# Optimization experiments

Measured on AMD Instinct MI355X. Metric: run time of the kernel, lower is better.

The kernel has to match this reference:

```python
import jax, jax.numpy as jnp
import numpy as np
import math

B, N, D, H = 4, 2048, 256, 4
DH = D // H
EPS = 1e-8


def setup_inputs() -> dict:
    key = jax.random.key(0)
    ks = jax.random.split(key, 8)
    x = jax.random.normal(ks[0], (B, N, D), dtype=jnp.float32)
    # RoPE rotation freqs: exp(i * pos * inv_freq), stored as (cos, sin) pairs -> [N, DH//2, 2]
    d2 = DH // 2
    inv_freq = 1.0 / (10000.0 ** (jnp.arange(d2, dtype=jnp.float32) / d2))
    ang = jnp.arange(N, dtype=jnp.float32)[:, None] * inv_freq[None, :]
    freqs = jnp.stack([jnp.cos(ang), jnp.sin(ang)], axis=-1)  # [N, d2, 2]
    s = 0.02
    g = jnp.ones((D,), dtype=jnp.float32)
    w_qkv = jax.random.normal(ks[1], (D, 3 * D), dtype=jnp.float32) * s
    b_qkv = jnp.zeros((3 * D,), dtype=jnp.float32)
    w_out = jax.random.normal(ks[2], (D, D), dtype=jnp.float32) * s
    b_out = jnp.zeros((D,), dtype=jnp.float32)
    w_gate = jax.random.normal(ks[3], (D, D), dtype=jnp.float32) * s
    b_gate = jnp.zeros((D,), dtype=jnp.float32)
    return {"x": x, "freqs": freqs, "g": g, "w_qkv": w_qkv, "b_qkv": b_qkv,
            "w_out": w_out, "b_out": b_out, "w_gate": w_gate, "b_gate": b_gate}


def _zcrmsnorm(x, g):
    x0 = x - jnp.mean(x, axis=-1, keepdims=True)
    rms = jnp.sqrt(jnp.mean(x0 * x0, axis=-1, keepdims=True) + EPS)
    return x0 / rms * g


def _rope(q, freqs):
    # q: [B,H,N,DH]; freqs: [N,DH//2,2] (cos,sin). Complex multiply on adjacent pairs.
    b, h, n, dh = q.shape
    qp = q.reshape(b, h, n, dh // 2, 2)
    cos = freqs[:n, :, 0][None, None]  # [1,1,N,d2]
    sin = freqs[:n, :, 1][None, None]
    q0, q1 = qp[..., 0], qp[..., 1]
    out = jnp.stack([q0 * cos - q1 * sin, q0 * sin + q1 * cos], axis=-1)
    return out.reshape(b, h, n, dh)


def reference(x, freqs, g, w_qkv, b_qkv, w_out, b_out, w_gate, b_gate):
    b, n, d = x.shape
    h = _zcrmsnorm(x, g)
    qkv = (h @ w_qkv + b_qkv).reshape(b, n, 3, H, DH)
    qkv = jnp.transpose(qkv, (2, 0, 3, 1, 4))  # [3,B,H,N,DH]
    q, k, v = qkv[0], qkv[1], qkv[2]
    q = _rope(q, freqs)
    k = _rope(k, freqs)
    scores = jnp.einsum('bhqd,bhkd->bhqk', q, k) / math.sqrt(DH)
    attn = jax.nn.softmax(scores, axis=-1)  # dropout is identity in eval
    y = jnp.einsum('bhqk,bhkd->bhqd', attn, v)
    y = jnp.transpose(y, (0, 2, 1, 3)).reshape(b, n, d)
    y = y @ w_out + b_out
    gate = jax.nn.sigmoid(h @ w_gate + b_gate)
    return x + gate * y
```

## Files before the change

kernel.cpp:

```cpp
#include <hip/hip_runtime.h>

typedef unsigned short u16;
typedef unsigned int u32;
typedef short short8 __attribute__((ext_vector_type(8)));
typedef float f32x4 __attribute__((ext_vector_type(4)));

#define B_ 4
#define N_ 2048
#define D_ 256
#define H_ 4
#define DH_ 64
#define BN_ 8192

__device__ inline float b2f(u16 u) {
    union { u32 i; float f; } v; v.i = ((u32)u) << 16; return v.f;
}
__device__ inline u16 f2b(float f) {
    union { float f; u32 i; } v; v.f = f;
    return (u16)((v.i + 0x8000u) >> 16);
}
__device__ inline u32 pkbf(float a, float b) {
    union { float f; u32 i; } ua, ub; ua.f = a; ub.f = b;
    return __builtin_amdgcn_perm(ub.i + 0x8000u, ua.i + 0x8000u, 0x07060302u);
}
__device__ inline f32x4 mfma16(short8 a, short8 b, f32x4 c) {
    return __builtin_amdgcn_mfma_f32_16x16x32_bf16(a, b, c, 0, 0, 0);
}

__device__ __forceinline__ void gemm_body(
    int bx, int by, int tid,
    const u16* __restrict__ A, const u16* __restrict__ BT,
    const float* __restrict__ bias, void* __restrict__ Cout,
    int Ntot)
{
    const int wave = tid >> 6, lane = tid & 63;
    const int ln15 = lane & 15, quad = lane >> 4;
    const int m0 = bx * 128 + (wave & 1) * 64;
    const int n0 = by * 128 + (wave >> 1) * 64;

    const f32x4 zero = {0.f, 0.f, 0.f, 0.f};
    f32x4 acc[4][4];
    #pragma unroll
    for (int i = 0; i < 4; ++i)
        #pragma unroll
        for (int j = 0; j < 4; ++j) acc[i][j] = zero;

    #pragma unroll
    for (int k0 = 0; k0 < 256; k0 += 32) {
        const int koff = k0 + quad * 8;
        short8 a[4], b[4];
        #pragma unroll
        for (int i = 0; i < 4; ++i)
            a[i] = *(const short8*)(A + (size_t)(m0 + i * 16 + ln15) * 256 + koff);
        #pragma unroll
        for (int j = 0; j < 4; ++j)
            b[j] = *(const short8*)(BT + (size_t)(n0 + j * 16 + ln15) * 256 + koff);
        #pragma unroll
        for (int i = 0; i < 4; ++i)
            #pragma unroll
            for (int j = 0; j < 4; ++j)
                acc[i][j] = mfma16(a[i], b[j], acc[i][j]);
    }

    #pragma unroll
    for (int i = 0; i < 4; ++i) {
        const int r = m0 + i * 16 + quad * 4;
        #pragma unroll
        for (int j = 0; j < 4; ++j) {
            const int c = n0 + j * 16 + ln15;
            const float bv = bias[c];
            #pragma unroll
            for (int rg = 0; rg < 4; ++rg) {
                const size_t idx = (size_t)(r + rg) * Ntot + c;
                ((u16*)Cout)[idx] = f2b(acc[i][j][rg] + bv);
            }
        }
    }
}

__device__ __forceinline__ void gemm_thin_body(
    int bx, int by, int tid,
    const u16* __restrict__ A, const u16* __restrict__ BT,
    const float* __restrict__ bias, void* __restrict__ Cout,
    const float* __restrict__ xin, const u16* __restrict__ gate,
    int mode)
{
    const int wave = tid >> 6, lane = tid & 63;
    const int ln15 = lane & 15, quad = lane >> 4;
    const int m0 = bx * 64 + (wave & 1) * 32;
    const int n0 = by * 64 + (wave >> 1) * 32;

    const f32x4 zero = {0.f, 0.f, 0.f, 0.f};
    f32x4 acc[2][2];
    #pragma unroll
    for (int i = 0; i < 2; ++i)
        #pragma unroll
        for (int j = 0; j < 2; ++j) acc[i][j] = zero;

    #pragma unroll
    for (int k0 = 0; k0 < 256; k0 += 32) {
        const int koff = k0 + quad * 8;
        short8 a[2], b[2];
        #pragma unroll
        for (int i = 0; i < 2; ++i)
            a[i] = *(const short8*)(A + (size_t)(m0 + i * 16 + ln15) * 256 + koff);
        #pragma unroll
        for (int j = 0; j < 2; ++j)
            b[j] = *(const short8*)(BT + (size_t)(n0 + j * 16 + ln15) * 256 + koff);
        #pragma unroll
        for (int i = 0; i < 2; ++i)
            #pragma unroll
            for (int j = 0; j < 2; ++j)
                acc[i][j] = mfma16(a[i], b[j], acc[i][j]);
    }

    #pragma unroll
    for (int i = 0; i < 2; ++i) {
        const int r = m0 + i * 16 + quad * 4;
        #pragma unroll
        for (int j = 0; j < 2; ++j) {
            const int c = n0 + j * 16 + ln15;
            const float bv = bias[c];
            #pragma unroll
            for (int rg = 0; rg < 4; ++rg) {
                const size_t idx = (size_t)(r + rg) * 256 + c;
                float v = acc[i][j][rg] + bv;
                if (mode == 1) {
                    ((u16*)Cout)[idx] = f2b(1.0f / (1.0f + __expf(-v)));
                } else {
                    ((float*)Cout)[idx] = xin[idx] + b2f(gate[idx]) * v;
                }
            }
        }
    }
}

__global__ __launch_bounds__(256) void gemm_ep(
    const u16* __restrict__ A, const u16* __restrict__ BT,
    const float* __restrict__ bias, void* __restrict__ Cout, int Ntot)
{
    gemm_body(blockIdx.x, blockIdx.y, threadIdx.x, A, BT, bias, Cout, Ntot);
}

__global__ __launch_bounds__(256) void gemm_thin(
    const u16* __restrict__ A, const u16* __restrict__ BT,
    const float* __restrict__ bias, void* __restrict__ Cout,
    const float* __restrict__ xin, const u16* __restrict__ gate, int mode)
{
    gemm_thin_body(blockIdx.x, blockIdx.y, threadIdx.x, A, BT, bias, Cout,
                   xin, gate, mode);
}

__global__ __launch_bounds__(256) void norm_transw_k(
    const float* __restrict__ x, const float* __restrict__ g, u16* __restrict__ h,
    const float* __restrict__ wqkv, const float* __restrict__ wout,
    const float* __restrict__ wgate,
    u16* __restrict__ wqkvT, u16* __restrict__ woutT, u16* __restrict__ wgateT)
{
    if (blockIdx.x < 2048) {
        const int wave = threadIdx.x >> 6, lane = threadIdx.x & 63;
        const int t = blockIdx.x * 4 + wave;
        const float4 u = *(const float4*)(x + (size_t)t * D_ + lane * 4);
        float s  = u.x + u.y + u.z + u.w;
        float s2 = u.x * u.x + u.y * u.y + u.z * u.z + u.w * u.w;
        #pragma unroll
        for (int m = 1; m < 64; m <<= 1) {
            s  += __shfl_xor(s, m);
            s2 += __shfl_xor(s2, m);
        }
        float mean = s * (1.0f / D_);
        float var  = s2 * (1.0f / D_) - mean * mean;
        float rinv = rsqrtf(var + 1e-8f);
        const float4 gv = *(const float4*)(g + lane * 4);
        uint2 o;
        o.x = pkbf((u.x - mean) * rinv * gv.x, (u.y - mean) * rinv * gv.y);
        o.y = pkbf((u.z - mean) * rinv * gv.z, (u.w - mean) * rinv * gv.w);
        *(uint2*)(h + (size_t)t * D_ + lane * 4) = o;
    } else {
        int idx = (blockIdx.x - 2048) * 256 + threadIdx.x;
        if (idx < 768 * 256) {
            int nn = idx >> 8, kk = idx & 255;
            wqkvT[idx] = f2b(wqkv[kk * 768 + nn]);
        }
        idx -= 768 * 256;
        if (idx >= 0 && idx < 256 * 256) {
            int nn = idx >> 8, kk = idx & 255;
            woutT[idx]  = f2b(wout[kk * 256 + nn]);
            wgateT[idx] = f2b(wgate[kk * 256 + nn]);
        }
    }
}

#define QSCALE 0.18033688f
__global__ __launch_bounds__(256) void rope_vt_gate_k(
    const u16* __restrict__ qkv, const float* __restrict__ freqs,
    u16* __restrict__ Q, u16* __restrict__ K, u16* __restrict__ VT,
    const u16* __restrict__ h, const u16* __restrict__ wgateT,
    const float* __restrict__ b_gate, u16* __restrict__ gatb)
{
    __shared__ __align__(16) u16 tile[64 * 65];
    const int blk = blockIdx.x;
    if (blk < 1024) {
        const int idx = blk * 256 + threadIdx.x;
        const int t = idx >> 5, rem = idx & 31;
        const int hh = rem >> 3, s8 = rem & 7;
        const int b = t >> 11, n = t & 2047;

        const float4 f0 = *(const float4*)(freqs + (size_t)n * 64 + s8 * 8);
        const float4 f1 = *(const float4*)(freqs + (size_t)n * 64 + s8 * 8 + 4);

        const u16* qp = qkv + (size_t)t * 768 + hh * 64 + s8 * 8;
        const uint4 qv = *(const uint4*)qp;
        const uint4 kv = *(const uint4*)(qp + 256);

        const size_t off = ((size_t)(b * H_ + hh) * N_ + n) * DH_ + s8 * 8;
        uint4 qo, ko;
        {
            float q0 = b2f((u16)(qv.x & 0xffff)), q1 = b2f((u16)(qv.x >> 16));
            float k0 = b2f((u16)(kv.x & 0xffff)), k1 = b2f((u16)(kv.x >> 16));
            qo.x = pkbf((q0 * f0.x - q1 * f0.y) * QSCALE, (q0 * f0.y + q1 * f0.x) * QSCALE);
            ko.x = pkbf(k0 * f0.x - k1 * f0.y, k0 * f0.y + k1 * f0.x);
        }
        {
            float q0 = b2f((u16)(qv.y & 0xffff)), q1 = b2f((u16)(qv.y >> 16));
            float k0 = b2f((u16)(kv.y & 0xffff)), k1 = b2f((u16)(kv.y >> 16));
            qo.y = pkbf((q0 * f0.z - q1 * f0.w) * QSCALE, (q0 * f0.w + q1 * f0.z) * QSCALE);
            ko.y = pkbf(k0 * f0.z - k1 * f0.w, k0 * f0.w + k1 * f0.z);
        }
        {
            float q0 = b2f((u16)(qv.z & 0xffff)), q1 = b2f((u16)(qv.z >> 16));
            float k0 = b2f((u16)(kv.z & 0xffff)), k1 = b2f((u16)(kv.z >> 16));
            qo.z = pkbf((q0 * f1.x - q1 * f1.y) * QSCALE, (q0 * f1.y + q1 * f1.x) * QSCALE);
            ko.z = pkbf(k0 * f1.x - k1 * f1.y, k0 * f1.y + k1 * f1.x);
        }
        {
            float q0 = b2f((u16)(qv.w & 0xffff)), q1 = b2f((u16)(qv.w >> 16));
            float k0 = b2f((u16)(kv.w & 0xffff)), k1 = b2f((u16)(kv.w >> 16));
            qo.w = pkbf((q0 * f1.z - q1 * f1.w) * QSCALE, (q0 * f1.w + q1 * f1.z) * QSCALE);
            ko.w = pkbf(k0 * f1.z - k1 * f1.w, k0 * f1.w + k1 * f1.z);
        }
        *(uint4*)(Q + off) = qo;
        *(uint4*)(K + off) = ko;
    } else if (blk < 1536) {
        const int id2 = blk - 1024;
        const int bh = id2 & 15;
        const int n0 = (id2 >> 4) * 64;
        const int b = bh >> 2, hh = bh & 3;
        #pragma unroll
        for (int rep = 0; rep < 16; ++rep) {
            int idx = rep * 256 + threadIdx.x;
            int nl = idx >> 6, dh = idx & 63;
            tile[dh * 65 + nl] = qkv[(size_t)(b * N_ + n0 + nl) * 768 + 512 + hh * 64 + dh];
        }
        __syncthreads();
        #pragma unroll
        for (int rep = 0; rep < 16; ++rep) {
            int idx = rep * 256 + threadIdx.x;
            int dh = idx >> 6, nl = idx & 63;
            VT[((size_t)bh * 64 + dh) * N_ + n0 + nl] = tile[dh * 65 + nl];
        }
    } else {
        const int id3 = blk - 1536;
        gemm_thin_body(id3 & 127, id3 >> 7, threadIdx.x, h, wgateT, b_gate,
                       (void*)gatb, (const float*)nullptr, (const u16*)nullptr, 1);
    }
}

__global__ __launch_bounds__(256) void attn_k(
    const u16* __restrict__ Q, const u16* __restrict__ K,
    const u16* __restrict__ VT, u16* __restrict__ yt)
{
    __shared__ __align__(16) u16 Ks[2][64][64];
    __shared__ __align__(16) u16 Vs[2][64][64];
    __shared__ __align__(16) u16 Pb[4][16 * 88];
    const int tid = threadIdx.x;
    const int wave = tid >> 6, lane = tid & 63;
    const int ln15 = lane & 15, quad = lane >> 4;
    const int id = blockIdx.x;
    const int bh = ((id & 7) << 1) | ((id >> 3) & 1);
    const int q0 = (id >> 4) * 64 + wave * 16;

    const u16* Qh = Q + (size_t)bh * N_ * DH_;
    const u16* Kh = K + (size_t)bh * N_ * DH_;
    const u16* Vh = VT + (size_t)bh * DH_ * N_;

    const short8 bq0 = *(const short8*)(Qh + (size_t)(q0 + ln15) * DH_ + quad * 8);
    const short8 bq1 = *(const short8*)(Qh + (size_t)(q0 + ln15) * DH_ + 32 + quad * 8);

    const f32x4 zero = {0.f, 0.f, 0.f, 0.f};
    f32x4 o[4];
    #pragma unroll
    for (int j = 0; j < 4; ++j) o[j] = zero;
    float lv = 0.f;
    u16* Pw = Pb[wave];

    const int srow = tid >> 2, sq4 = tid & 3;
    const int swr = (srow & 7) << 3;
    const int wc0 = (sq4 * 8) ^ swr;
    const int wc1 = (sq4 * 8 + 32) ^ swr;
    const int swl = (ln15 & 7) << 3;
    const int rc0 = (quad * 8) ^ swl;
    const int rc1 = (quad * 8 + 32) ^ swl;

    {
        uint4 k0 = *(const uint4*)(Kh + (size_t)srow * DH_ + sq4 * 8);
        uint4 k1 = *(const uint4*)(Kh + (size_t)srow * DH_ + (sq4 + 4) * 8);
        uint4 v0 = *(const uint4*)(Vh + (size_t)srow * N_ + sq4 * 8);
        uint4 v1 = *(const uint4*)(Vh + (size_t)srow * N_ + (sq4 + 4) * 8);
        *(uint4*)&Ks[0][srow][wc0] = k0;
        *(uint4*)&Ks[0][srow][wc1] = k1;
        *(uint4*)&Vs[0][srow][wc0] = v0;
        *(uint4*)&Vs[0][srow][wc1] = v1;
    }
    __syncthreads();

    int p = 0;
    for (int c = 0; c < 32; ++c) {
        const int ktn = (c + 1) * 64;
        uint4 k0, k1, v0, v1;
        const bool more = (c + 1 < 32);
        if (more) {
            k0 = *(const uint4*)(Kh + (size_t)(ktn + srow) * DH_ + sq4 * 8);
            k1 = *(const uint4*)(Kh + (size_t)(ktn + srow) * DH_ + (sq4 + 4) * 8);
            v0 = *(const uint4*)(Vh + (size_t)srow * N_ + ktn + sq4 * 8);
            v1 = *(const uint4*)(Vh + (size_t)srow * N_ + ktn + (sq4 + 4) * 8);
        }

        f32x4 st[4];
        #pragma unroll
        for (int c4 = 0; c4 < 4; ++c4) {
            short8 ka0 = *(const short8*)&Ks[p][c4 * 16 + ln15][rc0];
            short8 ka1 = *(const short8*)&Ks[p][c4 * 16 + ln15][rc1];
            st[c4] = mfma16(ka0, bq0, zero);
            st[c4] = mfma16(ka1, bq1, st[c4]);
        }
        f32x4 pr[4];
        float rs = 0.f;
        #pragma unroll
        for (int c4 = 0; c4 < 4; ++c4) {
            #pragma unroll
            for (int r = 0; r < 4; ++r) {
                pr[c4][r] = exp2f(st[c4][r]);
                rs += pr[c4][r];
            }
        }
        lv += rs;
        #pragma unroll
        for (int c4 = 0; c4 < 4; ++c4) {
            uint2 w;
            w.x = pkbf(pr[c4][0], pr[c4][1]);
            w.y = pkbf(pr[c4][2], pr[c4][3]);
            *(uint2*)(Pw + ln15 * 88 + c4 * 16 + quad * 4) = w;
        }
        asm volatile("s_waitcnt lgkmcnt(0)" ::: "memory");
        const short8 bp0 = *(const short8*)(Pw + ln15 * 88 + quad * 8);
        const short8 bp1 = *(const short8*)(Pw + ln15 * 88 + 32 + quad * 8);
        #pragma unroll
        for (int j = 0; j < 4; ++j) {
            short8 va0 = *(const short8*)&Vs[p][j * 16 + ln15][rc0];
            short8 va1 = *(const short8*)&Vs[p][j * 16 + ln15][rc1];
            o[j] = mfma16(va0, bp0, o[j]);
            o[j] = mfma16(va1, bp1, o[j]);
        }

        if (more) {
            *(uint4*)&Ks[p ^ 1][srow][wc0] = k0;
            *(uint4*)&Ks[p ^ 1][srow][wc1] = k1;
            *(uint4*)&Vs[p ^ 1][srow][wc0] = v0;
            *(uint4*)&Vs[p ^ 1][srow][wc1] = v1;
        }
        __syncthreads();
        p ^= 1;
    }

    lv += __shfl_xor(lv, 16);
    lv += __shfl_xor(lv, 32);
    const float rl = 1.0f / lv;
    const int b = bh >> 2, h = bh & 3;
    const size_t base = ((size_t)b * N_ + q0 + ln15) * D_ + h * 64;
    #pragma unroll
    for (int j = 0; j < 4; ++j) {
        uint2 w;
        w.x = pkbf(o[j][0] * rl, o[j][1] * rl);
        w.y = pkbf(o[j][2] * rl, o[j][3] * rl);
        *(uint2*)(yt + base + j * 16 + quad * 4) = w;
    }
}

extern "C" void kernel_launch(void* const* d_in, const int* in_sizes, int n_in,
                              void* d_out, int out_size, void* d_ws, size_t ws_size,
                              hipStream_t stream) {
    const float* x      = (const float*)d_in[0];
    const float* freqs  = (const float*)d_in[1];
    const float* g      = (const float*)d_in[2];
    const float* w_qkv  = (const float*)d_in[3];
    const float* b_qkv  = (const float*)d_in[4];
    const float* w_out  = (const float*)d_in[5];
    const float* b_out  = (const float*)d_in[6];
    const float* w_gate = (const float*)d_in[7];
    const float* b_gate = (const float*)d_in[8];
    float* out = (float*)d_out;

    char* ws = (char*)d_ws;
    size_t off = 0;
    auto carve = [&](size_t nelem) -> u16* {
        u16* p = (u16*)(ws + off);
        off += ((nelem * 2 + 255) / 256) * 256;
        return p;
    };
    u16* h      = carve((size_t)BN_ * D_);
    u16* qkv    = carve((size_t)BN_ * 768);
    u16* Qb     = carve((size_t)BN_ * D_);
    u16* Kb     = carve((size_t)BN_ * D_);
    u16* VT     = carve((size_t)BN_ * D_);
    u16* gatb   = carve((size_t)BN_ * D_);
    u16* wqkvT  = carve((size_t)768 * 256);
    u16* woutT  = carve((size_t)256 * 256);
    u16* wgateT = carve((size_t)256 * 256);
    u16* yt = qkv;

    hipLaunchKernelGGL(norm_transw_k, dim3(3072), dim3(256), 0, stream,
                       x, g, h, w_qkv, w_out, w_gate, wqkvT, woutT, wgateT);
    hipLaunchKernelGGL(gemm_ep, dim3(BN_ / 128, 6), dim3(256), 0, stream,
                       h, wqkvT, b_qkv, (void*)qkv, 768);
    hipLaunchKernelGGL(rope_vt_gate_k, dim3(2048), dim3(256), 0, stream,
                       qkv, freqs, Qb, Kb, VT, h, wgateT, b_gate, gatb);
    hipLaunchKernelGGL(attn_k, dim3(512), dim3(256), 0, stream,
                       Qb, Kb, VT, yt);
    hipLaunchKernelGGL(gemm_thin, dim3(128, 4), dim3(256), 0, stream,
                       yt, woutT, b_out, (void*)out, x, gatb, 2);
}
```

Before: 168.0 us.

## Split attention key range across two halves and merge partials in combine kernel

The attention kernel now uses 512-thread blocks covering 128 queries. Each block handles only half of the key sequence, which doubles the waves in flight per block and halves the loop length per wave. Unnormalized fp32 partial outputs and row sums are written to workspace, aliased over the dead h/qkv and weight buffers. A new combine kernel adds the two halves, normalizes, and writes bf16 output for the final GEMM. This trades an extra launch and about 16MB of fp32 partial traffic for more parallelism and latency hiding in attention.

```diff
diff --git a/kernel.cpp b/kernel.cpp
--- a/kernel.cpp
+++ b/kernel.cpp
@@ -266,19 +266,22 @@
     }
 }
 
-__global__ __launch_bounds__(256) void attn_k(
+__global__ __launch_bounds__(512, 4) void attn_k(
     const u16* __restrict__ Q, const u16* __restrict__ K,
-    const u16* __restrict__ VT, u16* __restrict__ yt)
+    const u16* __restrict__ VT, float* __restrict__ Op,
+    float* __restrict__ lvp)
 {
     __shared__ __align__(16) u16 Ks[2][64][64];
     __shared__ __align__(16) u16 Vs[2][64][64];
-    __shared__ __align__(16) u16 Pb[4][16 * 88];
+    __shared__ __align__(16) u16 Pb[8][16 * 88];
     const int tid = threadIdx.x;
     const int wave = tid >> 6, lane = tid & 63;
     const int ln15 = lane & 15, quad = lane >> 4;
     const int id = blockIdx.x;
-    const int bh = ((id & 7) << 1) | ((id >> 3) & 1);
-    const int q0 = (id >> 4) * 64 + wave * 16;
+    const int bh   = ((id & 7) << 1) | ((id >> 3) & 1);
+    const int half = (id >> 4) & 1;
+    const int q0   = (id >> 5) * 128 + wave * 16;
+    const int kt0  = half * 1024;
 
     const u16* Qh = Q + (size_t)bh * N_ * DH_;
     const u16* Kh = K + (size_t)bh * N_ * DH_;
@@ -294,36 +297,28 @@
     float lv = 0.f;
     u16* Pw = Pb[wave];
 
-    const int srow = tid >> 2, sq4 = tid & 3;
-    const int swr = (srow & 7) << 3;
-    const int wc0 = (sq4 * 8) ^ swr;
-    const int wc1 = (sq4 * 8 + 32) ^ swr;
+    const int srow = tid >> 3, sq8 = tid & 7;
+    const int wc = (sq8 * 8) ^ ((srow & 7) << 3);
     const int swl = (ln15 & 7) << 3;
     const int rc0 = (quad * 8) ^ swl;
     const int rc1 = (quad * 8 + 32) ^ swl;
 
     {
-        uint4 k0 = *(const uint4*)(Kh + (size_t)srow * DH_ + sq4 * 8);
-        uint4 k1 = *(const uint4*)(Kh + (size_t)srow * DH_ + (sq4 + 4) * 8);
-        uint4 v0 = *(const uint4*)(Vh + (size_t)srow * N_ + sq4 * 8);
-        uint4 v1 = *(const uint4*)(Vh + (size_t)srow * N_ + (sq4 + 4) * 8);
-        *(uint4*)&Ks[0][srow][wc0] = k0;
-        *(uint4*)&Ks[0][srow][wc1] = k1;
-        *(uint4*)&Vs[0][srow][wc0] = v0;
-        *(uint4*)&Vs[0][srow][wc1] = v1;
+        uint4 k0 = *(const uint4*)(Kh + (size_t)(kt0 + srow) * DH_ + sq8 * 8);
+        uint4 v0 = *(const uint4*)(Vh + (size_t)srow * N_ + kt0 + sq8 * 8);
+        *(uint4*)&Ks[0][srow][wc] = k0;
+        *(uint4*)&Vs[0][srow][wc] = v0;
     }
     __syncthreads();
 
     int p = 0;
-    for (int c = 0; c < 32; ++c) {
-        const int ktn = (c + 1) * 64;
-        uint4 k0, k1, v0, v1;
-        const bool more = (c + 1 < 32);
+    for (int c = 0; c < 16; ++c) {
+        const int ktn = kt0 + (c + 1) * 64;
+        uint4 k0, v0;
+        const bool more = (c + 1 < 16);
         if (more) {
-            k0 = *(const uint4*)(Kh + (size_t)(ktn + srow) * DH_ + sq4 * 8);
-            k1 = *(const uint4*)(Kh + (size_t)(ktn + srow) * DH_ + (sq4 + 4) * 8);
-            v0 = *(const uint4*)(Vh + (size_t)srow * N_ + ktn + sq4 * 8);
-            v1 = *(const uint4*)(Vh + (size_t)srow * N_ + ktn + (sq4 + 4) * 8);
+            k0 = *(const uint4*)(Kh + (size_t)(ktn + srow) * DH_ + sq8 * 8);
+            v0 = *(const uint4*)(Vh + (size_t)srow * N_ + ktn + sq8 * 8);
         }
 
         f32x4 st[4];
@@ -364,10 +359,8 @@
         }
 
         if (more) {
-            *(uint4*)&Ks[p ^ 1][srow][wc0] = k0;
-            *(uint4*)&Ks[p ^ 1][srow][wc1] = k1;
-            *(uint4*)&Vs[p ^ 1][srow][wc0] = v0;
-            *(uint4*)&Vs[p ^ 1][srow][wc1] = v1;
+            *(uint4*)&Ks[p ^ 1][srow][wc] = k0;
+            *(uint4*)&Vs[p ^ 1][srow][wc] = v0;
         }
         __syncthreads();
         p ^= 1;
@@ -375,16 +368,37 @@
 
     lv += __shfl_xor(lv, 16);
     lv += __shfl_xor(lv, 32);
-    const float rl = 1.0f / lv;
+    const size_t rowo = ((size_t)(half * 16 + bh) * N_ + q0 + ln15) * DH_;
+    #pragma unroll
+    for (int j = 0; j < 4; ++j) {
+        float4 w4 = {o[j][0], o[j][1], o[j][2], o[j][3]};
+        *(float4*)(Op + rowo + j * 16 + quad * 4) = w4;
+    }
+    if (quad == 0) lvp[(size_t)(half * 16 + bh) * N_ + q0 + ln15] = lv;
+}
+
+__global__ __launch_bounds__(256) void combine_k(
+    const float* __restrict__ Op, const float* __restrict__ lvp,
+    u16* __restrict__ yt)
+{
+    const int t = blockIdx.x * 256 + threadIdx.x;
+    const int dh0 = (t & 7) * 8;
+    const int q   = (t >> 3) & 2047;
+    const int bh  = t >> 14;
+    const size_t o0 = ((size_t)bh * N_ + q) * DH_ + dh0;
+    const size_t o1 = o0 + (size_t)16 * N_ * DH_;
+    const float4 a0 = *(const float4*)(Op + o0);
+    const float4 a1 = *(const float4*)(Op + o0 + 4);
+    const float4 c0 = *(const float4*)(Op + o1);
+    const float4 c1 = *(const float4*)(Op + o1 + 4);
+    const float rl = 1.0f / (lvp[(size_t)bh * N_ + q] + lvp[(size_t)(16 + bh) * N_ + q]);
+    uint4 w;
+    w.x = pkbf((a0.x + c0.x) * rl, (a0.y + c0.y) * rl);
+    w.y = pkbf((a0.z + c0.z) * rl, (a0.w + c0.w) * rl);
+    w.z = pkbf((a1.x + c1.x) * rl, (a1.y + c1.y) * rl);
+    w.w = pkbf((a1.z + c1.z) * rl, (a1.w + c1.w) * rl);
     const int b = bh >> 2, h = bh & 3;
-    const size_t base = ((size_t)b * N_ + q0 + ln15) * D_ + h * 64;
-    #pragma unroll
-    for (int j = 0; j < 4; ++j) {
-        uint2 w;
-        w.x = pkbf(o[j][0] * rl, o[j][1] * rl);
-        w.y = pkbf(o[j][2] * rl, o[j][3] * rl);
-        *(uint2*)(yt + base + j * 16 + quad * 4) = w;
-    }
+    *(uint4*)(yt + ((size_t)b * N_ + q) * D_ + h * 64 + dh0) = w;
 }
 
 extern "C" void kernel_launch(void* const* d_in, const int* in_sizes, int n_in,
@@ -417,7 +431,9 @@
     u16* wqkvT  = carve((size_t)768 * 256);
     u16* woutT  = carve((size_t)256 * 256);
     u16* wgateT = carve((size_t)256 * 256);
-    u16* yt = qkv;
+    float* Op  = (float*)ws;
+    float* lvp = (float*)wqkvT;
+    u16*   yt  = Qb;
 
     hipLaunchKernelGGL(norm_transw_k, dim3(3072), dim3(256), 0, stream,
                        x, g, h, w_qkv, w_out, w_gate, wqkvT, woutT, wgateT);
@@ -425,8 +441,10 @@
                        h, wqkvT, b_qkv, (void*)qkv, 768);
     hipLaunchKernelGGL(rope_vt_gate_k, dim3(2048), dim3(256), 0, stream,
                        qkv, freqs, Qb, Kb, VT, h, wgateT, b_gate, gatb);
-    hipLaunchKernelGGL(attn_k, dim3(512), dim3(256), 0, stream,
-                       Qb, Kb, VT, yt);
+    hipLaunchKernelGGL(attn_k, dim3(512), dim3(512), 0, stream,
+                       Qb, Kb, VT, Op, lvp);
+    hipLaunchKernelGGL(combine_k, dim3(1024), dim3(256), 0, stream,
+                       Op, lvp, yt);
     hipLaunchKernelGGL(gemm_thin, dim3(128, 4), dim3(256), 0, stream,
                        yt, woutT, b_out, (void*)out, x, gatb, 2);
 }
```

Result: no change. 165.9 us (-1.2%).
